# Optimization experiments

Measured on AMD Instinct MI355X. Metric: run time of the kernel, lower is better.

The kernel has to match this reference:

```python
import jax, jax.numpy as jnp
import numpy as np

S = 16384   # num src nodes
D = 16384   # num dst nodes
FS = 128    # src feature len
FD = 128    # dst feature len
R = 50.0    # dist threshold (m)
L = 2005.0  # box side so avg degree ~ 32
LN_EPS = 1e-5


def setup_inputs() -> dict:
    rng = np.random.default_rng(0)
    src_pos_np = rng.uniform(0.0, L, (S, 2)).astype(np.float32)
    dst_pos_np = rng.uniform(0.0, L, (D, 2)).astype(np.float32)
    # radius-graph edge construction (data-dependent, done once outside jit)
    es, ed = [], []
    CH = 2048
    for i in range(0, S, CH):
        d = np.linalg.norm(src_pos_np[i:i + CH, None, :] - dst_pos_np[None, :, :], axis=-1)
        si, di = np.nonzero(d <= R)
        es.append((si + i).astype(np.int32))
        ed.append(di.astype(np.int32))
    edge_src_idx = jnp.asarray(np.concatenate(es))
    edge_dst_idx = jnp.asarray(np.concatenate(ed))

    key = jax.random.key(0)
    ks = jax.random.split(key, 12)
    w = lambda k, shape: (jax.random.normal(k, shape, jnp.float32) * 0.02)
    return {
        'src_node_features': jax.random.normal(ks[0], (S, FS), jnp.float32),
        'src_node_pos': jnp.asarray(src_pos_np),
        'dst_node_features': jax.random.normal(ks[1], (D, FD), jnp.float32),
        'dst_node_pos': jnp.asarray(dst_pos_np),
        'src_w': w(ks[2], (FS, FS)), 'src_b': jnp.zeros((FS,), jnp.float32),
        'dst_w': w(ks[3], (FD, FD)), 'dst_b': jnp.zeros((FD,), jnp.float32),
        'dist_w': w(ks[4], (2, FD)), 'dist_b': jnp.zeros((FD,), jnp.float32),
        'edge_w1': w(ks[5], (FS + FD + FD, FD)), 'edge_b1': jnp.zeros((FD,), jnp.float32),
        'edge_w2': w(ks[6], (FD, FD)), 'edge_b2': jnp.zeros((FD,), jnp.float32),
        'ln_g': jnp.ones((FD,), jnp.float32), 'ln_b': jnp.zeros((FD,), jnp.float32),
        'out_w': w(ks[7], (FD, FD)), 'out_b': jnp.zeros((FD,), jnp.float32),
        'edge_src_idx': edge_src_idx,
        'edge_dst_idx': edge_dst_idx,
    }


def reference(src_node_features, src_node_pos, dst_node_features, dst_node_pos,
              src_w, src_b, dst_w, dst_b, dist_w, dist_b,
              edge_w1, edge_b1, edge_w2, edge_b2, ln_g, ln_b, out_w, out_b,
              edge_src_idx, edge_dst_idx):
    # node encoders: Linear + ReLU
    src_enc = jax.nn.relu(src_node_features @ src_w + src_b)   # [S, FS]
    dst_enc = jax.nn.relu(dst_node_features @ dst_w + dst_b)   # [D, FD]
    # gather per-edge
    e_src = src_enc[edge_src_idx]                               # [E, FS]
    e_dst = dst_enc[edge_dst_idx]                               # [E, FD]
    e_dpos = src_node_pos[edge_src_idx] - dst_node_pos[edge_dst_idx]  # [E, 2]
    e_dist = jax.nn.relu(e_dpos @ dist_w + dist_b)              # [E, FD]
    # edge MLP: Linear-ReLU-Linear on concat [E, FS+FD+FD]
    e_in = jnp.concatenate([e_src, e_dist, e_dst], axis=-1)
    e_out = jax.nn.relu(e_in @ edge_w1 + edge_b1) @ edge_w2 + edge_b2  # [E, FD]
    # scatter-add to destination nodes
    agg = dst_enc + jax.ops.segment_sum(e_out, edge_dst_idx, num_segments=D)
    # LayerNorm + ReLU + Linear + residual + ReLU
    mu = jnp.mean(agg, axis=-1, keepdims=True)
    var = jnp.mean(jnp.square(agg - mu), axis=-1, keepdims=True)
    ln = (agg - mu) * jax.lax.rsqrt(var + LN_EPS) * ln_g + ln_b
    h = jax.nn.relu(ln) @ out_w + out_b + dst_node_features
    return jax.nn.relu(h)
```

## Files before the change

kernel.cpp:

```cpp
#include <hip/hip_runtime.h>

typedef unsigned short ushort_t;
typedef unsigned int uint_t;
typedef short bhalf8 __attribute__((ext_vector_type(8)));
typedef float f32x4 __attribute__((ext_vector_type(4)));

__device__ __forceinline__ float b2f(ushort_t u) {
    union { uint_t i; float f; } v; v.i = ((uint_t)u) << 16; return v.f;
}
__device__ __forceinline__ ushort_t f2b(float f) {
    union { float f; uint_t i; } v; v.f = f;
    uint_t r = v.i + 0x7fffu + ((v.i >> 16) & 1u);
    return (ushort_t)(r >> 16);
}
__device__ __forceinline__ uint_t f2u(float f) {
    union { float f; uint_t i; } v; v.f = f; return v.i;
}
__device__ __forceinline__ uint_t pack_trunc(float lo, float hi) {
    return (f2u(lo) >> 16) | (f2u(hi) & 0xffff0000u);
}
__device__ __forceinline__ uint_t addpack_trunc(uint_t a, uint_t b) {
    union { uint_t i; float f; } t0, t1, s0, s1;
    t0.i = a << 16;          s0.i = b << 16;
    t1.i = a & 0xffff0000u;  s1.i = b & 0xffff0000u;
    return pack_trunc(t0.f + s0.f, t1.f + s1.f);
}

__global__ __launch_bounds__(256) void prep_kernel(
    const float* __restrict__ wsrc, const float* __restrict__ wdst,
    const float* __restrict__ w2,   const float* __restrict__ wout,
    const float* __restrict__ w1,
    ushort_t* __restrict__ msrc, ushort_t* __restrict__ mdst,
    ushort_t* __restrict__ m2,   ushort_t* __restrict__ mout,
    ushort_t* __restrict__ m1a,  ushort_t* __restrict__ m1b,
    ushort_t* __restrict__ m1c,
    const int* __restrict__ edi, int E, int* __restrict__ deg,
    float* __restrict__ hsum, int countB, int zeroB, int Dn)
{
    int b = blockIdx.x, tid = threadIdx.x;
    if (b < 56) {
        const float* ins[7] = { wsrc, wdst, w2, wout, w1, w1 + 128*128, w1 + 256*128 };
        ushort_t* outs[7]   = { msrc, mdst, m2, mout, m1a, m1b, m1c };
        int mat = b >> 3;
        const float* in = ins[mat];
        ushort_t* out = outs[mat];
        int flat = (b & 7)*256 + tid;
        int nt = flat >> 8, rem = flat & 255;
        int ks = rem >> 6, lane = rem & 63;
        int q = lane >> 4, m = lane & 15;
        #pragma unroll
        for (int j = 0; j < 8; ++j)
            out[flat*8 + j] = f2b(in[(ks*32 + q*8 + j)*128 + nt*16 + m]);
    } else if (b < 56 + countB) {
        int i = (b - 56)*256 + tid;
        if (i < E) atomicAdd(&deg[edi[i]], 1);
    } else {
        int zb = b - 56 - countB;
        float4* h4 = (float4*)hsum;
        int total4 = Dn*32;
        for (int i = zb*256 + tid; i < total4; i += zeroB*256)
            h4[i] = make_float4(0.f, 0.f, 0.f, 0.f);
    }
}

__global__ __launch_bounds__(256) void enc2_kernel(
    const float* __restrict__ src_feat, const float* __restrict__ dst_feat,
    const ushort_t* __restrict__ msrc, const ushort_t* __restrict__ mdst,
    const ushort_t* __restrict__ m1a,  const ushort_t* __restrict__ m1c,
    const float* __restrict__ src_b,   const float* __restrict__ dst_b,
    const float* __restrict__ b1,
    ushort_t* __restrict__ Csrc, ushort_t* __restrict__ Cdst,
    ushort_t* __restrict__ dst_enc,
    const int* __restrict__ deg, int* __restrict__ nxt, int Dn,
    int Sb, int Db)
{
    int tid = threadIdx.x, blk = blockIdx.x;

    if (blk == Sb + Db) {
        __shared__ int sums[256];
        int per = Dn >> 8;
        const int4* d4 = (const int4*)(deg + tid*per);
        int4 v[16]; int s = 0;
        #pragma unroll
        for (int k = 0; k < 16; ++k) { v[k] = d4[k]; s += v[k].x + v[k].y + v[k].z + v[k].w; }
        sums[tid] = s;
        __syncthreads();
        for (int off = 1; off < 256; off <<= 1) {
            int x = (tid >= off) ? sums[tid - off] : 0;
            __syncthreads();
            sums[tid] += x;
            __syncthreads();
        }
        int run = sums[tid] - s;
        int4* n4 = (int4*)(nxt + tid*per);
        #pragma unroll
        for (int k = 0; k < 16; ++k) {
            int4 o;
            o.x = run; run += v[k].x;
            o.y = run; run += v[k].y;
            o.z = run; run += v[k].z;
            o.w = run; run += v[k].w;
            n4[k] = o;
        }
        return;
    }

    __shared__ ushort_t A_l[64*136];
    __shared__ ushort_t E_l[64*136];
    __shared__ float b_l[128];
    __shared__ float b2_l[128];

    const float* A; const ushort_t *W1m, *W2m; const float* bias;
    ushort_t *outC, *outEnc; int rowbase; const float* bias2;
    if (blk < Sb) { A = src_feat; W1m = msrc; W2m = m1a; bias = src_b;
                    outC = Csrc; outEnc = nullptr; rowbase = blk*64; bias2 = nullptr; }
    else          { A = dst_feat; W1m = mdst; W2m = m1c; bias = dst_b;
                    outC = Cdst; outEnc = dst_enc; rowbase = (blk - Sb)*64; bias2 = b1; }

    const float4* A4 = (const float4*)A;
    for (int i = tid; i < 2048; i += 256) {
        int r = i >> 5, c = i & 31;
        float4 v = A4[(size_t)(rowbase + r)*32 + c];
        uint2 u;
        u.x = (uint_t)f2b(v.x) | ((uint_t)f2b(v.y) << 16);
        u.y = (uint_t)f2b(v.z) | ((uint_t)f2b(v.w) << 16);
        *(uint2*)(A_l + r*136 + c*4) = u;
    }
    if (tid < 128) { b_l[tid] = bias[tid]; b2_l[tid] = bias2 ? bias2[tid] : 0.f; }
    __syncthreads();

    int lane = tid & 63, w = tid >> 6, q = lane >> 4, m = lane & 15;
    const bhalf8* Wv1 = (const bhalf8*)W1m;
    f32x4 acc[4][2] = {};
    #pragma unroll
    for (int ks = 0; ks < 4; ++ks) {
        bhalf8 bf0 = Wv1[((2*w)*4 + ks)*64 + lane];
        bhalf8 bf1 = Wv1[((2*w+1)*4 + ks)*64 + lane];
        #pragma unroll
        for (int mt = 0; mt < 4; ++mt) {
            bhalf8 a = *(const bhalf8*)(A_l + (mt*16 + m)*136 + ks*32 + q*8);
            acc[mt][0] = __builtin_amdgcn_mfma_f32_16x16x32_bf16(a, bf0, acc[mt][0], 0, 0, 0);
            acc[mt][1] = __builtin_amdgcn_mfma_f32_16x16x32_bf16(a, bf1, acc[mt][1], 0, 0, 0);
        }
    }
    #pragma unroll
    for (int mt = 0; mt < 4; ++mt)
    #pragma unroll
    for (int nt = 0; nt < 2; ++nt)
    #pragma unroll
    for (int reg = 0; reg < 4; ++reg) {
        int col = w*32 + nt*16 + m;
        int row = mt*16 + q*4 + reg;
        ushort_t e = f2b(fmaxf(acc[mt][nt][reg] + b_l[col], 0.f));
        E_l[row*136 + col] = e;
        if (outEnc) outEnc[(size_t)(rowbase + row)*128 + col] = e;
    }
    __syncthreads();

    const bhalf8* Wv2 = (const bhalf8*)W2m;
    f32x4 acc2[4][2] = {};
    #pragma unroll
    for (int ks = 0; ks < 4; ++ks) {
        bhalf8 bf0 = Wv2[((2*w)*4 + ks)*64 + lane];
        bhalf8 bf1 = Wv2[((2*w+1)*4 + ks)*64 + lane];
        #pragma unroll
        for (int mt = 0; mt < 4; ++mt) {
            bhalf8 a = *(const bhalf8*)(E_l + (mt*16 + m)*136 + ks*32 + q*8);
            acc2[mt][0] = __builtin_amdgcn_mfma_f32_16x16x32_bf16(a, bf0, acc2[mt][0], 0, 0, 0);
            acc2[mt][1] = __builtin_amdgcn_mfma_f32_16x16x32_bf16(a, bf1, acc2[mt][1], 0, 0, 0);
        }
    }
    #pragma unroll
    for (int mt = 0; mt < 4; ++mt)
    #pragma unroll
    for (int nt = 0; nt < 2; ++nt)
    #pragma unroll
    for (int reg = 0; reg < 4; ++reg) {
        int col = w*32 + nt*16 + m;
        int row = mt*16 + q*4 + reg;
        outC[(size_t)(rowbase + row)*128 + col] = f2b(acc2[mt][nt][reg] + b2_l[col]);
    }
}

__global__ __launch_bounds__(256) void fill_sorted(
    const int* __restrict__ esi, const int* __restrict__ edi, int E,
    int* __restrict__ nxt, int2* __restrict__ spair)
{
    int i = blockIdx.x*256 + threadIdx.x;
    if (i < E) {
        int s = esi[i], d = edi[i];
        int p = atomicAdd(&nxt[d], 1);
        spair[p] = make_int2(s, d);
    }
}

__global__ __launch_bounds__(256, 4) void edge_kernel(
    const ushort_t* __restrict__ Csrc, const ushort_t* __restrict__ Cdst,
    const float* __restrict__ src_pos, const float* __restrict__ dst_pos,
    const int2* __restrict__ spair, int E,
    const ushort_t* __restrict__ w1bm,
    const float* __restrict__ dist_w, const float* __restrict__ dist_b,
    float* __restrict__ hsum)
{
    __shared__ char pool[34816];
    __shared__ int s_l[64], d_l[64], dv_l[64], bnd_l[64], dofs_l[64];
    __shared__ float dx_l[64], dy_l[64];
    __shared__ float dw0_l[128], dw1_l[128], db_l[128];

    ushort_t* X = (ushort_t*)pool;
    ushort_t* G = (ushort_t*)(pool + 17408);
    float* H = (float*)pool;

    int tid = threadIdx.x, blk = blockIdx.x;

    if (tid < 64) {
        int slot = blk*64 + tid;
        if (slot < E) {
            int2 pr = spair[slot];
            s_l[tid] = pr.x; d_l[tid] = pr.y; dv_l[tid] = pr.y;
            float2 sp = ((const float2*)src_pos)[pr.x];
            float2 dp = ((const float2*)dst_pos)[pr.y];
            dx_l[tid] = sp.x - dp.x;
            dy_l[tid] = sp.y - dp.y;
        } else {
            s_l[tid] = 0; d_l[tid] = -1; dv_l[tid] = 0;
            dx_l[tid] = 0.f; dy_l[tid] = 0.f;
        }
    }
    if (tid < 128) {
        dw0_l[tid] = dist_w[tid];
        dw1_l[tid] = dist_w[128 + tid];
        db_l[tid]  = dist_b[tid];
    }
    __syncthreads();

    if (tid < 64) {
        int d = d_l[tid];
        int dn = (tid < 63) ? d_l[tid + 1] : -2;
        bnd_l[tid] = (tid == 31) || (tid == 63) || (dn != d);
        dofs_l[tid] = (d >= 0) ? d*128 : -1;
    }
    const uint4* cs4 = (const uint4*)Csrc;
    const uint4* cd4 = (const uint4*)Cdst;
    for (int i = tid; i < 1024; i += 256) {
        int r = i >> 4, c = i & 15;
        uint4 a = cs4[(size_t)s_l[r]*16 + c];
        uint4 b = cd4[(size_t)dv_l[r]*16 + c];
        uint4 u;
        u.x = addpack_trunc(a.x, b.x);
        u.y = addpack_trunc(a.y, b.y);
        u.z = addpack_trunc(a.z, b.z);
        u.w = addpack_trunc(a.w, b.w);
        *(uint4*)(G + r*136 + c*8) = u;
    }
    for (int i = tid; i < 4096; i += 256) {
        int r = i >> 6, j2 = (i & 63)*2;
        float dx = dx_l[r], dy = dy_l[r];
        float v0 = fmaxf(fmaf(dx, dw0_l[j2],   fmaf(dy, dw1_l[j2],   db_l[j2])),   0.f);
        float v1 = fmaxf(fmaf(dx, dw0_l[j2+1], fmaf(dy, dw1_l[j2+1], db_l[j2+1])), 0.f);
        *(uint_t*)(X + r*136 + j2) = pack_trunc(v0, v1);
    }
    __syncthreads();

    int lane = tid & 63, w = tid >> 6, q = lane >> 4, m = lane & 15;
    f32x4 acc[4][2] = {};
    const bhalf8* Wv = (const bhalf8*)w1bm;
    #pragma unroll
    for (int ks = 0; ks < 4; ++ks) {
        bhalf8 bf0 = Wv[((2*w)*4 + ks)*64 + lane];
        bhalf8 bf1 = Wv[((2*w+1)*4 + ks)*64 + lane];
        #pragma unroll
        for (int mt = 0; mt < 4; ++mt) {
            bhalf8 a = *(const bhalf8*)(X + (mt*16 + m)*136 + ks*32 + q*8);
            acc[mt][0] = __builtin_amdgcn_mfma_f32_16x16x32_bf16(a, bf0, acc[mt][0], 0, 0, 0);
            acc[mt][1] = __builtin_amdgcn_mfma_f32_16x16x32_bf16(a, bf1, acc[mt][1], 0, 0, 0);
        }
    }
    __syncthreads();

    #pragma unroll
    for (int mt = 0; mt < 2; ++mt)
    #pragma unroll
    for (int reg = 0; reg < 4; ++reg) {
        int row = mt*16 + q*4 + reg;
        #pragma unroll
        for (int nt = 0; nt < 2; ++nt) {
            int col = w*32 + nt*16 + m;
            H[row*132 + col] = fmaxf(acc[mt][nt][reg] + b2f(G[row*136 + col]), 0.f);
        }
    }
    float gv[2][4][2];
    #pragma unroll
    for (int mt = 2; mt < 4; ++mt)
    #pragma unroll
    for (int reg = 0; reg < 4; ++reg) {
        int row = mt*16 + q*4 + reg;
        #pragma unroll
        for (int nt = 0; nt < 2; ++nt)
            gv[mt-2][reg][nt] = b2f(G[row*136 + w*32 + nt*16 + m]);
    }
    __syncthreads();

    #pragma unroll
    for (int mt = 2; mt < 4; ++mt)
    #pragma unroll
    for (int reg = 0; reg < 4; ++reg) {
        int row = mt*16 + q*4 + reg;
        #pragma unroll
        for (int nt = 0; nt < 2; ++nt) {
            int col = w*32 + nt*16 + m;
            H[row*132 + col] = fmaxf(acc[mt][nt][reg] + gv[mt-2][reg][nt], 0.f);
        }
    }
    __syncthreads();

    {
        int j = tid & 127, h = tid >> 7;
        int rend = h*32 + 32;
        float a = 0.f;
        for (int r = h*32; r < rend; ++r) {
            a += H[r*132 + j];
            if (bnd_l[r]) {
                int ofs = dofs_l[r];
                if (ofs >= 0) atomicAdd(&hsum[(size_t)ofs + j], a);
                a = 0.f;
            }
        }
    }
}

__global__ __launch_bounds__(256) void aggfinal_kernel(
    const float* __restrict__ hsum, const ushort_t* __restrict__ w2m,
    const float* __restrict__ b2, const int* __restrict__ deg,
    const ushort_t* __restrict__ dst_enc, const float* __restrict__ ln_g,
    const float* __restrict__ ln_b, const ushort_t* __restrict__ moutm,
    const float* __restrict__ out_b, const float* __restrict__ dst_feat,
    float* __restrict__ out)
{
    __shared__ char buf[64*132*4];
    __shared__ ushort_t act_l[64*136];
    __shared__ float b2_l[128], g_l[128], bl_l[128], ob_l[128];
    __shared__ int deg_l[64];
    __shared__ float ps[64][4], ps2[64][4], mu_l[64], inv_l[64];

    ushort_t* A_l = (ushort_t*)buf;
    float* Y = (float*)buf;
    int tid = threadIdx.x, blk = blockIdx.x;

    const float4* hv = (const float4*)hsum;
    for (int i = tid; i < 1024; i += 256) {
        int r = i >> 4, c = i & 15;
        size_t base = (size_t)(blk*64 + r)*32 + c*2;
        float4 p0 = hv[base], p1 = hv[base + 1];
        uint4 u;
        u.x = (uint_t)f2b(p0.x) | ((uint_t)f2b(p0.y) << 16);
        u.y = (uint_t)f2b(p0.z) | ((uint_t)f2b(p0.w) << 16);
        u.z = (uint_t)f2b(p1.x) | ((uint_t)f2b(p1.y) << 16);
        u.w = (uint_t)f2b(p1.z) | ((uint_t)f2b(p1.w) << 16);
        *(uint4*)(A_l + r*136 + c*8) = u;
    }
    if (tid < 128) { b2_l[tid] = b2[tid]; g_l[tid] = ln_g[tid];
                     bl_l[tid] = ln_b[tid]; ob_l[tid] = out_b[tid]; }
    if (tid < 64) deg_l[tid] = deg[blk*64 + tid];
    __syncthreads();

    int lane = tid & 63, w = tid >> 6, q = lane >> 4, m = lane & 15;
    f32x4 acc[4][2] = {};
    const bhalf8* Wv = (const bhalf8*)w2m;
    #pragma unroll
    for (int ks = 0; ks < 4; ++ks) {
        bhalf8 bf0 = Wv[((2*w)*4 + ks)*64 + lane];
        bhalf8 bf1 = Wv[((2*w+1)*4 + ks)*64 + lane];
        #pragma unroll
        for (int mt = 0; mt < 4; ++mt) {
            bhalf8 a = *(const bhalf8*)(A_l + (mt*16 + m)*136 + ks*32 + q*8);
            acc[mt][0] = __builtin_amdgcn_mfma_f32_16x16x32_bf16(a, bf0, acc[mt][0], 0, 0, 0);
            acc[mt][1] = __builtin_amdgcn_mfma_f32_16x16x32_bf16(a, bf1, acc[mt][1], 0, 0, 0);
        }
    }
    __syncthreads();

    #pragma unroll
    for (int mt = 0; mt < 4; ++mt)
    #pragma unroll
    for (int nt = 0; nt < 2; ++nt)
    #pragma unroll
    for (int reg = 0; reg < 4; ++reg) {
        int col = w*32 + nt*16 + m;
        int rowl = mt*16 + q*4 + reg;
        size_t grow = (size_t)blk*64 + rowl;
        float v = acc[mt][nt][reg] + (float)deg_l[rowl]*b2_l[col] + b2f(dst_enc[grow*128 + col]);
        Y[rowl*132 + col] = v;
    }
    __syncthreads();

    {
        int r = tid >> 2, t4 = tid & 3;
        float s = 0.f, s2 = 0.f;
        for (int jj = 0; jj < 32; ++jj) {
            float v = Y[r*132 + t4*32 + jj];
            s += v; s2 += v*v;
        }
        ps[r][t4] = s; ps2[r][t4] = s2;
    }
    __syncthreads();
    if (tid < 64) {
        int r = tid;
        float sum = ps[r][0] + ps[r][1] + ps[r][2] + ps[r][3];
        float sum2 = ps2[r][0] + ps2[r][1] + ps2[r][2] + ps2[r][3];
        float mu = sum / 128.f;
        float var = sum2 / 128.f - mu*mu;
        mu_l[r] = mu;
        inv_l[r] = 1.0f / sqrtf(var + 1e-5f);
    }
    __syncthreads();
    for (int i = tid; i < 4096; i += 256) {
        int r = i >> 6, j2 = (i & 63)*2;
        float v0 = fmaxf((Y[r*132 + j2]   - mu_l[r]) * inv_l[r] * g_l[j2]   + bl_l[j2],   0.f);
        float v1 = fmaxf((Y[r*132 + j2+1] - mu_l[r]) * inv_l[r] * g_l[j2+1] + bl_l[j2+1], 0.f);
        *(uint_t*)(act_l + r*136 + j2) = (uint_t)f2b(v0) | ((uint_t)f2b(v1) << 16);
    }
    __syncthreads();

    f32x4 acc2[4][2] = {};
    const bhalf8* Wo = (const bhalf8*)moutm;
    #pragma unroll
    for (int ks = 0; ks < 4; ++ks) {
        bhalf8 bf0 = Wo[((2*w)*4 + ks)*64 + lane];
        bhalf8 bf1 = Wo[((2*w+1)*4 + ks)*64 + lane];
        #pragma unroll
        for (int mt = 0; mt < 4; ++mt) {
            bhalf8 a = *(const bhalf8*)(act_l + (mt*16 + m)*136 + ks*32 + q*8);
            acc2[mt][0] = __builtin_amdgcn_mfma_f32_16x16x32_bf16(a, bf0, acc2[mt][0], 0, 0, 0);
            acc2[mt][1] = __builtin_amdgcn_mfma_f32_16x16x32_bf16(a, bf1, acc2[mt][1], 0, 0, 0);
        }
    }
    #pragma unroll
    for (int mt = 0; mt < 4; ++mt)
    #pragma unroll
    for (int nt = 0; nt < 2; ++nt)
    #pragma unroll
    for (int reg = 0; reg < 4; ++reg) {
        int col = w*32 + nt*16 + m;
        size_t row = (size_t)blk*64 + mt*16 + q*4 + reg;
        float v = acc2[mt][nt][reg] + ob_l[col] + dst_feat[row*128 + col];
        out[row*128 + col] = fmaxf(v, 0.f);
    }
}

extern "C" void kernel_launch(void* const* d_in, const int* in_sizes, int n_in,
                              void* d_out, int out_size, void* d_ws, size_t ws_size,
                              hipStream_t stream)
{
    const float* src_feat = (const float*)d_in[0];
    const float* src_pos  = (const float*)d_in[1];
    const float* dst_feat = (const float*)d_in[2];
    const float* dst_pos  = (const float*)d_in[3];
    const float* src_w    = (const float*)d_in[4];
    const float* src_b    = (const float*)d_in[5];
    const float* dst_w    = (const float*)d_in[6];
    const float* dst_b    = (const float*)d_in[7];
    const float* dist_w   = (const float*)d_in[8];
    const float* dist_b   = (const float*)d_in[9];
    const float* w1       = (const float*)d_in[10];
    const float* b1       = (const float*)d_in[11];
    const float* w2       = (const float*)d_in[12];
    const float* b2       = (const float*)d_in[13];
    const float* ln_g     = (const float*)d_in[14];
    const float* ln_b     = (const float*)d_in[15];
    const float* out_w    = (const float*)d_in[16];
    const float* out_b    = (const float*)d_in[17];
    const int* esi        = (const int*)d_in[18];
    const int* edi        = (const int*)d_in[19];
    int E = in_sizes[18];
    int S = in_sizes[0] / 128;
    int D = in_sizes[2] / 128;

    char* ws = (char*)d_ws;
    size_t off = 0;
    auto alloc = [&](size_t bytes) { char* p = ws + off; off += (bytes + 511) & ~(size_t)511; return p; };
    ushort_t* Csrc    = (ushort_t*)alloc((size_t)S*128*2);
    ushort_t* Cdst    = (ushort_t*)alloc((size_t)D*128*2);
    ushort_t* dst_enc = (ushort_t*)alloc((size_t)D*128*2);
    float*    hsum    = (float*)   alloc((size_t)D*128*4);
    ushort_t* msrc    = (ushort_t*)alloc(128*128*2);
    ushort_t* mdst    = (ushort_t*)alloc(128*128*2);
    ushort_t* m2      = (ushort_t*)alloc(128*128*2);
    ushort_t* mout    = (ushort_t*)alloc(128*128*2);
    ushort_t* m1a     = (ushort_t*)alloc(128*128*2);
    ushort_t* m1b     = (ushort_t*)alloc(128*128*2);
    ushort_t* m1c     = (ushort_t*)alloc(128*128*2);
    int*      deg     = (int*)     alloc((size_t)D*4);
    int*      nxt     = (int*)     alloc((size_t)D*4);
    int2*     spair   = (int2*)    alloc((size_t)E*8);

    hipMemsetAsync(deg, 0, (size_t)D*4, stream);

    int countB = (E + 255)/256;
    int zeroB = 256;
    prep_kernel<<<56 + countB + zeroB, 256, 0, stream>>>(
        src_w, dst_w, w2, out_w, w1,
        msrc, mdst, m2, mout, m1a, m1b, m1c,
        edi, E, deg, hsum, countB, zeroB, D);

    int Sb = S/64, Db = D/64;
    enc2_kernel<<<Sb + Db + 1, 256, 0, stream>>>(
        src_feat, dst_feat, msrc, mdst, m1a, m1c, src_b, dst_b, b1,
        Csrc, Cdst, dst_enc, deg, nxt, D, Sb, Db);

    fill_sorted<<<(E + 255)/256, 256, 0, stream>>>(esi, edi, E, nxt, spair);

    edge_kernel<<<(E + 63)/64, 256, 0, stream>>>(
        Csrc, Cdst, src_pos, dst_pos, spair, E,
        m1b, dist_w, dist_b, hsum);

    aggfinal_kernel<<<Db, 256, 0, stream>>>(
        hsum, m2, b2, deg, dst_enc, ln_g, ln_b,
        mout, out_b, dst_feat, (float*)d_out);
}
```

Measured before the change: 234.2 us.

## Stage edge hidden in transposed bf16 LDS and coalesce encoder stores

The edge kernel now stores the pre-activation MFMA output as a column-major bf16 tile instead of a row-major fp32 tile. The bias add and ReLU move into the segmented-reduction loop, and segment boundaries come from a ballot bitmask. This halves LDS usage and removes the two-phase write with its extra barrier. The node encoder kernel writes its outputs through LDS as coalesced uint4 stores, and several fp32-to-bf16 conversions switch from round-to-nearest to truncation, which adds some rounding error.

```diff
diff --git a/kernel.cpp b/kernel.cpp
--- a/kernel.cpp
+++ b/kernel.cpp
@@ -7,6 +7,9 @@
 
 __device__ __forceinline__ float b2f(ushort_t u) {
     union { uint_t i; float f; } v; v.i = ((uint_t)u) << 16; return v.f;
+}
+__device__ __forceinline__ float u2f(uint_t u) {
+    union { uint_t i; float f; } v; v.i = u; return v.f;
 }
 __device__ __forceinline__ ushort_t f2b(float f) {
     union { float f; uint_t i; } v; v.f = f;
@@ -122,8 +125,8 @@
         int r = i >> 5, c = i & 31;
         float4 v = A4[(size_t)(rowbase + r)*32 + c];
         uint2 u;
-        u.x = (uint_t)f2b(v.x) | ((uint_t)f2b(v.y) << 16);
-        u.y = (uint_t)f2b(v.z) | ((uint_t)f2b(v.w) << 16);
+        u.x = pack_trunc(v.x, v.y);
+        u.y = pack_trunc(v.z, v.w);
         *(uint2*)(A_l + r*136 + c*4) = u;
     }
     if (tid < 128) { b_l[tid] = bias[tid]; b2_l[tid] = bias2 ? bias2[tid] : 0.f; }
@@ -151,11 +154,16 @@
     for (int reg = 0; reg < 4; ++reg) {
         int col = w*32 + nt*16 + m;
         int row = mt*16 + q*4 + reg;
-        ushort_t e = f2b(fmaxf(acc[mt][nt][reg] + b_l[col], 0.f));
-        E_l[row*136 + col] = e;
-        if (outEnc) outEnc[(size_t)(rowbase + row)*128 + col] = e;
-    }
-    __syncthreads();
+        E_l[row*136 + col] = f2b(fmaxf(acc[mt][nt][reg] + b_l[col], 0.f));
+    }
+    __syncthreads();
+
+    if (outEnc) {
+        for (int i = tid; i < 1024; i += 256) {
+            int r = i >> 4, c = i & 15;
+            ((uint4*)outEnc)[(size_t)(rowbase + r)*16 + c] = *(const uint4*)(E_l + r*136 + c*8);
+        }
+    }
 
     const bhalf8* Wv2 = (const bhalf8*)W2m;
     f32x4 acc2[4][2] = {};
@@ -178,7 +186,12 @@
     for (int reg = 0; reg < 4; ++reg) {
         int col = w*32 + nt*16 + m;
         int row = mt*16 + q*4 + reg;
-        outC[(size_t)(rowbase + row)*128 + col] = f2b(acc2[mt][nt][reg] + b2_l[col]);
+        A_l[row*136 + col] = f2b(acc2[mt][nt][reg] + b2_l[col]);
+    }
+    __syncthreads();
+    for (int i = tid; i < 1024; i += 256) {
+        int r = i >> 4, c = i & 15;
+        ((uint4*)outC)[(size_t)(rowbase + r)*16 + c] = *(const uint4*)(A_l + r*136 + c*8);
     }
 }
 
@@ -202,30 +215,32 @@
     const float* __restrict__ dist_w, const float* __restrict__ dist_b,
     float* __restrict__ hsum)
 {
-    __shared__ char pool[34816];
-    __shared__ int s_l[64], d_l[64], dv_l[64], bnd_l[64], dofs_l[64];
+    __shared__ char pool[17408];
+    __shared__ ushort_t G[64*136];
+    __shared__ int s_l[64], d_l[64], dofs_l[64];
+    __shared__ uint_t bndmask[2];
     __shared__ float dx_l[64], dy_l[64];
     __shared__ float dw0_l[128], dw1_l[128], db_l[128];
 
-    ushort_t* X = (ushort_t*)pool;
-    ushort_t* G = (ushort_t*)(pool + 17408);
-    float* H = (float*)pool;
+    ushort_t* X  = (ushort_t*)pool;
+    ushort_t* Hc = (ushort_t*)pool;
 
     int tid = threadIdx.x, blk = blockIdx.x;
 
     if (tid < 64) {
         int slot = blk*64 + tid;
+        int s = 0, d = -1;
+        float dx = 0.f, dy = 0.f;
         if (slot < E) {
             int2 pr = spair[slot];
-            s_l[tid] = pr.x; d_l[tid] = pr.y; dv_l[tid] = pr.y;
-            float2 sp = ((const float2*)src_pos)[pr.x];
-            float2 dp = ((const float2*)dst_pos)[pr.y];
-            dx_l[tid] = sp.x - dp.x;
-            dy_l[tid] = sp.y - dp.y;
-        } else {
-            s_l[tid] = 0; d_l[tid] = -1; dv_l[tid] = 0;
-            dx_l[tid] = 0.f; dy_l[tid] = 0.f;
-        }
+            s = pr.x; d = pr.y;
+            float2 sp = ((const float2*)src_pos)[s];
+            float2 dp = ((const float2*)dst_pos)[d];
+            dx = sp.x - dp.x; dy = sp.y - dp.y;
+        }
+        s_l[tid] = s; d_l[tid] = d;
+        dofs_l[tid] = (d >= 0) ? d*128 : -1;
+        dx_l[tid] = dx; dy_l[tid] = dy;
     }
     if (tid < 128) {
         dw0_l[tid] = dist_w[tid];
@@ -237,15 +252,19 @@
     if (tid < 64) {
         int d = d_l[tid];
         int dn = (tid < 63) ? d_l[tid + 1] : -2;
-        bnd_l[tid] = (tid == 31) || (tid == 63) || (dn != d);
-        dofs_l[tid] = (d >= 0) ? d*128 : -1;
-    }
+        bool bnd = (tid == 31) || (tid == 63) || (dn != d);
+        unsigned long long mask = __ballot(bnd);
+        if (tid == 0) { bndmask[0] = (uint_t)mask; bndmask[1] = (uint_t)(mask >> 32); }
+    }
+
     const uint4* cs4 = (const uint4*)Csrc;
     const uint4* cd4 = (const uint4*)Cdst;
-    for (int i = tid; i < 1024; i += 256) {
+    #pragma unroll
+    for (int k = 0; k < 4; ++k) {
+        int i = tid + k*256;
         int r = i >> 4, c = i & 15;
         uint4 a = cs4[(size_t)s_l[r]*16 + c];
-        uint4 b = cd4[(size_t)dv_l[r]*16 + c];
+        uint4 b = cd4[(size_t)max(d_l[r], 0)*16 + c];
         uint4 u;
         u.x = addpack_trunc(a.x, b.x);
         u.y = addpack_trunc(a.y, b.y);
@@ -279,51 +298,42 @@
     __syncthreads();
 
     #pragma unroll
-    for (int mt = 0; mt < 2; ++mt)
-    #pragma unroll
-    for (int reg = 0; reg < 4; ++reg) {
-        int row = mt*16 + q*4 + reg;
-        #pragma unroll
-        for (int nt = 0; nt < 2; ++nt) {
-            int col = w*32 + nt*16 + m;
-            H[row*132 + col] = fmaxf(acc[mt][nt][reg] + b2f(G[row*136 + col]), 0.f);
-        }
-    }
-    float gv[2][4][2];
-    #pragma unroll
-    for (int mt = 2; mt < 4; ++mt)
-    #pragma unroll
-    for (int reg = 0; reg < 4; ++reg) {
-        int row = mt*16 + q*4 + reg;
-        #pragma unroll
-        for (int nt = 0; nt < 2; ++nt)
-            gv[mt-2][reg][nt] = b2f(G[row*136 + w*32 + nt*16 + m]);
-    }
-    __syncthreads();
-
-    #pragma unroll
-    for (int mt = 2; mt < 4; ++mt)
-    #pragma unroll
-    for (int reg = 0; reg < 4; ++reg) {
-        int row = mt*16 + q*4 + reg;
-        #pragma unroll
-        for (int nt = 0; nt < 2; ++nt) {
-            int col = w*32 + nt*16 + m;
-            H[row*132 + col] = fmaxf(acc[mt][nt][reg] + gv[mt-2][reg][nt], 0.f);
-        }
+    for (int mt = 0; mt < 4; ++mt)
+    #pragma unroll
+    for (int nt = 0; nt < 2; ++nt) {
+        int col = w*32 + nt*16 + m;
+        int row0 = mt*16 + q*4;
+        uint2 u;
+        u.x = pack_trunc(acc[mt][nt][0], acc[mt][nt][1]);
+        u.y = pack_trunc(acc[mt][nt][2], acc[mt][nt][3]);
+        *(uint2*)(Hc + col*68 + row0) = u;
     }
     __syncthreads();
 
     {
         int j = tid & 127, h = tid >> 7;
-        int rend = h*32 + 32;
+        uint_t mask = bndmask[h];
+        const ushort_t* Hcol = Hc + j*68 + h*32;
+        int rbase = h*32;
         float a = 0.f;
-        for (int r = h*32; r < rend; ++r) {
-            a += H[r*132 + j];
-            if (bnd_l[r]) {
-                int ofs = dofs_l[r];
-                if (ofs >= 0) atomicAdd(&hsum[(size_t)ofs + j], a);
-                a = 0.f;
+        #pragma unroll
+        for (int k8 = 0; k8 < 8; ++k8) {
+            uint2 hp = *(const uint2*)(Hcol + k8*4);
+            float hv[4];
+            hv[0] = u2f(hp.x << 16);
+            hv[1] = u2f(hp.x & 0xffff0000u);
+            hv[2] = u2f(hp.y << 16);
+            hv[3] = u2f(hp.y & 0xffff0000u);
+            #pragma unroll
+            for (int t = 0; t < 4; ++t) {
+                int r = rbase + k8*4 + t;
+                float g = b2f(G[r*136 + j]);
+                a += fmaxf(hv[t] + g, 0.f);
+                if ((mask >> (k8*4 + t)) & 1u) {
+                    int ofs = dofs_l[r];
+                    if (ofs >= 0) atomicAdd(&hsum[(size_t)ofs + j], a);
+                    a = 0.f;
+                }
             }
         }
     }
@@ -353,10 +363,10 @@
         size_t base = (size_t)(blk*64 + r)*32 + c*2;
         float4 p0 = hv[base], p1 = hv[base + 1];
         uint4 u;
-        u.x = (uint_t)f2b(p0.x) | ((uint_t)f2b(p0.y) << 16);
-        u.y = (uint_t)f2b(p0.z) | ((uint_t)f2b(p0.w) << 16);
-        u.z = (uint_t)f2b(p1.x) | ((uint_t)f2b(p1.y) << 16);
-        u.w = (uint_t)f2b(p1.z) | ((uint_t)f2b(p1.w) << 16);
+        u.x = pack_trunc(p0.x, p0.y);
+        u.y = pack_trunc(p0.z, p0.w);
+        u.z = pack_trunc(p1.x, p1.y);
+        u.w = pack_trunc(p1.z, p1.w);
         *(uint4*)(A_l + r*136 + c*8) = u;
     }
     if (tid < 128) { b2_l[tid] = b2[tid]; g_l[tid] = ln_g[tid];
```

Measured after the change: 224.6 us. 4.1% less time.
